# Optimization experiments

Measured on AMD Instinct MI355X. Metric: run time of the kernel, lower is better.

## Reference

```python
import jax, jax.numpy as jnp
import numpy as np

DIM = 768
NUM_HEADS = 12
HIDDEN = int(DIM * 4.0)
EPS = 1e-5


def setup_inputs() -> dict:
    key = jax.random.key(0)
    ks = jax.random.split(key, 8)
    s = lambda k, shape, scale=0.02: jax.random.normal(k, shape, dtype=jnp.float32) * scale
    return {
        "x": jax.random.normal(ks[0], (8, 1024, DIM), dtype=jnp.float32),
        "ln1_g": jnp.ones((DIM,), jnp.float32),
        "ln1_b": jnp.zeros((DIM,), jnp.float32),
        "qkv_w": s(ks[1], (DIM, 3 * DIM)),
        "qkv_b": jnp.zeros((3 * DIM,), jnp.float32),
        "proj_w": s(ks[2], (DIM, DIM)),
        "proj_b": jnp.zeros((DIM,), jnp.float32),
        "ln2_g": jnp.ones((DIM,), jnp.float32),
        "ln2_b": jnp.zeros((DIM,), jnp.float32),
        "fc1_w": s(ks[3], (DIM, HIDDEN)),
        "fc1_b": jnp.zeros((HIDDEN,), jnp.float32),
        "fc2_w": s(ks[4], (HIDDEN, DIM)),
        "fc2_b": jnp.zeros((DIM,), jnp.float32),
    }


def layer_norm(x, g, b):
    mu = jnp.mean(x, axis=-1, keepdims=True)
    var = jnp.mean(jnp.square(x - mu), axis=-1, keepdims=True)
    return (x - mu) * jax.lax.rsqrt(var + EPS) * g + b


def reference(x, ln1_g, ln1_b, qkv_w, qkv_b, proj_w, proj_b,
              ln2_g, ln2_b, fc1_w, fc1_b, fc2_w, fc2_b):
    B, N, C = x.shape
    H = NUM_HEADS
    Dh = C // H
    scale = Dh ** -0.5

    # --- Attention (pre-norm) ---
    h = layer_norm(x, ln1_g, ln1_b)
    qkv = h @ qkv_w + qkv_b                       # [B, N, 3C]
    qkv = qkv.reshape(B, N, 3, H, Dh)
    q, k, v = qkv[:, :, 0], qkv[:, :, 1], qkv[:, :, 2]  # [B, N, H, Dh]
    attn = jnp.einsum("bqhd,bkhd->bhqk", q, k) * scale  # [B, H, N, N]
    attn = jax.nn.softmax(attn, axis=-1)
    o = jnp.einsum("bhqk,bkhd->bqhd", attn, v).reshape(B, N, C)
    x = x + (o @ proj_w + proj_b)

    # --- MLP (pre-norm) ---
    h = layer_norm(x, ln2_g, ln2_b)
    h = jax.nn.gelu(h @ fc1_w + fc1_b, approximate=False)  # torch nn.GELU = exact erf
    x = x + (h @ fc2_w + fc2_b)
    return x
```

## Files before the change

kernel.cpp:

```cpp
#include <hip/hip_runtime.h>
#include <hip/hip_bf16.h>
#include <cstdint>

using f32x4   = __attribute__((ext_vector_type(4))) float;
using f32x16  = __attribute__((ext_vector_type(16))) float;
using bf16x8  = __attribute__((ext_vector_type(8))) short;

__device__ inline ushort f2bf(float f) {
    union { float f; uint u; } x; x.f = f;
    uint u = x.u;
    return (ushort)((u + 0x7FFFu + ((u >> 16) & 1u)) >> 16);
}

__device__ inline void gload16(const ushort* g, ushort* lds) {
    __builtin_amdgcn_global_load_lds(
        (const __attribute__((address_space(1))) unsigned int*)g,
        (__attribute__((address_space(3))) unsigned int*)lds, 16, 0, 0);
}

__device__ inline void transpose_body(const float* __restrict__ w,
                                      ushort* __restrict__ wt,
                                      int K, int N, int bx, int by,
                                      float (*tile)[33]) {
    const int bn = bx * 32, bk = by * 32;
    const int tx = threadIdx.x & 31, ty = threadIdx.x >> 5;
#pragma unroll
    for (int i = 0; i < 32; i += 8)
        tile[ty + i][tx] = w[(size_t)(bk + ty + i) * N + bn + tx];
    __syncthreads();
#pragma unroll
    for (int i = 0; i < 32; i += 8)
        wt[(size_t)(bn + ty + i) * K + bk + tx] = f2bf(tile[tx][ty + i]);
}

__device__ inline void ln_body(const float* __restrict__ x,
                               const float* __restrict__ g,
                               const float* __restrict__ b,
                               ushort* __restrict__ out, int row,
                               float* sa, float* sb) {
    const float* xr = x + (size_t)row * 768;
    const int t = threadIdx.x;
    float v0 = xr[t], v1 = xr[t + 256], v2 = xr[t + 512];
    float s  = v0 + v1 + v2;
    float sq = v0 * v0 + v1 * v1 + v2 * v2;
#pragma unroll
    for (int off = 32; off > 0; off >>= 1) {
        s  += __shfl_down(s, off);
        sq += __shfl_down(sq, off);
    }
    const int wv = t >> 6, lane = t & 63;
    if (lane == 0) { sa[wv] = s; sb[wv] = sq; }
    __syncthreads();
    s  = sa[0] + sa[1] + sa[2] + sa[3];
    sq = sb[0] + sb[1] + sb[2] + sb[3];
    const float mu   = s * (1.0f / 768.0f);
    const float var  = sq * (1.0f / 768.0f) - mu * mu;
    const float rstd = rsqrtf(var + 1e-5f);
    ushort* orow = out + (size_t)row * 768;
    orow[t]       = f2bf((v0 - mu) * rstd * g[t]       + b[t]);
    orow[t + 256] = f2bf((v1 - mu) * rstd * g[t + 256] + b[t + 256]);
    orow[t + 512] = f2bf((v2 - mu) * rstd * g[t + 512] + b[t + 512]);
}

__global__ __launch_bounds__(256) void prep(const float* __restrict__ qkv_w,
                                            const float* __restrict__ proj_w,
                                            const float* __restrict__ fc1_w,
                                            const float* __restrict__ fc2_w,
                                            ushort* __restrict__ qkv_wt,
                                            ushort* __restrict__ proj_wt,
                                            ushort* __restrict__ fc1_wt,
                                            ushort* __restrict__ fc2_wt,
                                            const float* __restrict__ x,
                                            const float* __restrict__ ln1_g,
                                            const float* __restrict__ ln1_b,
                                            ushort* __restrict__ hb) {
    __shared__ float tile[32][33];
    __shared__ float sa[4], sb[4];
    int blk = blockIdx.x;
    if (blk < 1728)      transpose_body(qkv_w, qkv_wt, 768, 2304, blk % 72, blk / 72, tile);
    else if (blk < 2304) { blk -= 1728; transpose_body(proj_w, proj_wt, 768, 768,  blk % 24, blk / 24, tile); }
    else if (blk < 4608) { blk -= 2304; transpose_body(fc1_w,  fc1_wt,  768, 3072, blk % 96, blk / 96, tile); }
    else if (blk < 6912) { blk -= 4608; transpose_body(fc2_w,  fc2_wt,  3072, 768, blk % 24, blk / 24, tile); }
    else                 ln_body(x, ln1_g, ln1_b, hb, blk - 6912, sa, sb);
}

__global__ __launch_bounds__(256) void ln_bf16(const float* __restrict__ x,
                                               const float* __restrict__ g,
                                               const float* __restrict__ b,
                                               ushort* __restrict__ out) {
    __shared__ float sa[4], sb[4];
    ln_body(x, g, b, out, blockIdx.x, sa, sb);
}

template <int EPI, int SWZ>
__global__ __launch_bounds__(256) void gemm_bt(const ushort* __restrict__ A,
                                               const ushort* __restrict__ Bt,
                                               const float* __restrict__ bias,
                                               const float* __restrict__ resid,
                                               void* __restrict__ out,
                                               void* __restrict__ out2,
                                               int M, int N, int K, int gx) {
    __shared__ ushort As[3][128 * 32];
    __shared__ ushort Bs[3][128 * 32];
    int bm, bn;
    if (SWZ) {
        const int bid = blockIdx.x;
        const int x = bid & 7, s = bid >> 3;
        bm = ((s / gx) * 8 + x) * 128;
        bn = (s % gx) * 128;
    } else {
        bm = blockIdx.y * 128;
        bn = blockIdx.x * 128;
    }
    const int t    = threadIdx.x;
    const int lane = t & 63;
    const int w    = t >> 6;
    const int wr   = w >> 1, wc = w & 1;
    const int lr   = lane >> 4, lc = lane & 15;

    const f32x4 fzero = {0.f, 0.f, 0.f, 0.f};
    f32x4 acc[4][4];
#pragma unroll
    for (int ai = 0; ai < 4; ++ai)
#pragma unroll
        for (int bj = 0; bj < 4; ++bj) acc[ai][bj] = fzero;

    const int srow = lane >> 2;
    const int sk8  = (lane & 3) * 8;
    const ushort* Ag0 = A  + (size_t)(bm + w * 16 + srow) * K + sk8;
    const ushort* Ag1 = Ag0 + (size_t)64 * K;
    const ushort* Bg0 = Bt + (size_t)(bn + w * 16 + srow) * K + sk8;
    const ushort* Bg1 = Bg0 + (size_t)64 * K;
    const int lo0 = (w * 16) * 32, lo1 = (64 + w * 16) * 32;

    const int nt = K >> 5;
    auto issue = [&](int tile, int buf) {
        const int kb = tile << 5;
        gload16(Ag0 + kb, &As[buf][lo0]);
        gload16(Ag1 + kb, &As[buf][lo1]);
        gload16(Bg0 + kb, &Bs[buf][lo0]);
        gload16(Bg1 + kb, &Bs[buf][lo1]);
    };
    issue(0, 0);
    if (nt > 1) issue(1, 1);

    for (int tk = 0; tk < nt; ++tk) {
        if (tk + 1 < nt) asm volatile("s_waitcnt vmcnt(4)" ::: "memory");
        else             asm volatile("s_waitcnt vmcnt(0)" ::: "memory");
        __builtin_amdgcn_sched_barrier(0);
        __builtin_amdgcn_s_barrier();
        __builtin_amdgcn_sched_barrier(0);
        if (tk + 2 < nt) issue(tk + 2, (tk + 2) % 3);
        const int cb = tk % 3;
        bf16x8 af[4], bf[4];
#pragma unroll
        for (int ai = 0; ai < 4; ++ai)
            af[ai] = *(const bf16x8*)&As[cb][(wr * 64 + ai * 16 + lc) * 32 + lr * 8];
#pragma unroll
        for (int bj = 0; bj < 4; ++bj)
            bf[bj] = *(const bf16x8*)&Bs[cb][(wc * 64 + bj * 16 + lc) * 32 + lr * 8];
#pragma unroll
        for (int ai = 0; ai < 4; ++ai)
#pragma unroll
            for (int bj = 0; bj < 4; ++bj)
                acc[ai][bj] = __builtin_amdgcn_mfma_f32_16x16x32_bf16(af[ai], bf[bj],
                                                                      acc[ai][bj], 0, 0, 0);
    }

#pragma unroll
    for (int ai = 0; ai < 4; ++ai) {
#pragma unroll
        for (int bj = 0; bj < 4; ++bj) {
            int col  = bn + wc * 64 + bj * 16 + lc;
            float bs = bias[col];
            if (EPI == 3 && col >= 1536) {
                int row0 = bm + wr * 64 + ai * 16 + lr * 4;
                int bb   = row0 >> 10, key0 = row0 & 1023;
                int c    = col - 1536;
                int h    = c >> 6, d = c & 63;
                ushort4 pk;
                pk.x = f2bf(acc[ai][bj][0] + bs);
                pk.y = f2bf(acc[ai][bj][1] + bs);
                pk.z = f2bf(acc[ai][bj][2] + bs);
                pk.w = f2bf(acc[ai][bj][3] + bs);
                *(ushort4*)((ushort*)out2 +
                            ((size_t)(bb * 12 + h) * 64 + d) * 1024 + key0) = pk;
                continue;
            }
            const float qsc = (EPI == 3 && col < 768) ? 0.125f : 1.0f;
#pragma unroll
            for (int j = 0; j < 4; ++j) {
                int row   = bm + wr * 64 + ai * 16 + lr * 4 + j;
                float val = acc[ai][bj][j] + bs;
                if (EPI == 1) {
                    val += resid[(size_t)row * N + col];
                    ((float*)out)[(size_t)row * N + col] = val;
                } else if (EPI == 2) {
                    val = 0.5f * val * (1.0f + erff(val * 0.70710678118f));
                    ((ushort*)out)[(size_t)row * N + col] = f2bf(val);
                } else {
                    ((ushort*)out)[(size_t)row * N + col] = f2bf(val * qsc);
                }
            }
        }
    }
}

__global__ __launch_bounds__(256) void attn_mfma(const ushort* __restrict__ qkv,
                                                 const ushort* __restrict__ vT,
                                                 ushort* __restrict__ outb) {
    __shared__ ushort Kls[64 * 72];
    __shared__ ushort Vtls[64 * 72];

    const int bid = blockIdx.x;
    const int b   = bid / 96;
    const int rem = bid % 96;
    const int h   = rem >> 3;
    const int qc  = rem & 7;
    const int t    = threadIdx.x;
    const int w    = t >> 6;
    const int lane = t & 63;
    const int l31  = lane & 31;
    const int hi   = lane >> 5;
    const int q0   = qc * 128 + w * 32;
    const size_t bbase = (size_t)b * 1024;
    const ushort* vTh = vT + ((size_t)(b * 12 + h) * 64) * 1024;

    bf16x8 qb[4];
    {
        const size_t qrow = (bbase + q0 + l31) * 2304 + h * 64;
#pragma unroll
        for (int dblk = 0; dblk < 4; ++dblk)
            qb[dblk] = *(const bf16x8*)(qkv + qrow + dblk * 16 + hi * 8);
    }

    f32x16 O[2];
#pragma unroll
    for (int ob = 0; ob < 2; ++ob)
#pragma unroll
        for (int r = 0; r < 16; ++r) O[ob][r] = 0.0f;
    float l = 0.0f;

    for (int kt = 0; kt < 16; ++kt) {
        const int k0 = kt * 64;
        __syncthreads();
#pragma unroll
        for (int i = 0; i < 2; ++i) {
            int idx = t + i * 256;
            int key = idx >> 3, seg = idx & 7;
            uint4 u = *(const uint4*)(qkv + (bbase + k0 + key) * 2304 + 768 +
                                      h * 64 + seg * 8);
            *(uint4*)&Kls[key * 72 + seg * 8] = u;
        }
#pragma unroll
        for (int i = 0; i < 2; ++i) {
            int idx = t + i * 256;
            int d = idx >> 3, seg = idx & 7;
            uint4 u = *(const uint4*)(vTh + (size_t)d * 1024 + k0 + seg * 8);
            *(uint4*)&Vtls[d * 72 + seg * 8] = u;
        }
        __syncthreads();

        f32x16 s[2];
#pragma unroll
        for (int kb = 0; kb < 2; ++kb) {
            f32x16 acc;
#pragma unroll
            for (int r = 0; r < 16; ++r) acc[r] = 0.0f;
#pragma unroll
            for (int dblk = 0; dblk < 4; ++dblk) {
                bf16x8 ka = *(const bf16x8*)&Kls[(kb * 32 + l31) * 72 + dblk * 16 + hi * 8];
                acc = __builtin_amdgcn_mfma_f32_32x32x16_bf16(ka, qb[dblk], acc, 0, 0, 0);
            }
            s[kb] = acc;
        }

        float psum = 0.0f;
#pragma unroll
        for (int kb = 0; kb < 2; ++kb)
#pragma unroll
            for (int r = 0; r < 16; ++r) {
                float p = __expf(s[kb][r]);
                s[kb][r] = p;
                psum += p;
            }
        psum += __shfl_xor(psum, 32);
        l += psum;

        bf16x8 pb[4];
#pragma unroll
        for (int kb16 = 0; kb16 < 4; ++kb16) {
            const int sb = kb16 >> 1, r0 = (kb16 & 1) * 8;
            uint own01 = (uint)f2bf(s[sb][r0 + 0]) | ((uint)f2bf(s[sb][r0 + 1]) << 16);
            uint own23 = (uint)f2bf(s[sb][r0 + 2]) | ((uint)f2bf(s[sb][r0 + 3]) << 16);
            uint own45 = (uint)f2bf(s[sb][r0 + 4]) | ((uint)f2bf(s[sb][r0 + 5]) << 16);
            uint own67 = (uint)f2bf(s[sb][r0 + 6]) | ((uint)f2bf(s[sb][r0 + 7]) << 16);
            uint sw01 = __shfl_xor(own01, 32);
            uint sw23 = __shfl_xor(own23, 32);
            uint sw45 = __shfl_xor(own45, 32);
            uint sw67 = __shfl_xor(own67, 32);
            uint d0 = hi ? sw45 : own01;
            uint d1 = hi ? sw67 : own23;
            uint d2 = hi ? own45 : sw01;
            uint d3 = hi ? own67 : sw23;
            union { uint u[4]; bf16x8 v; } cvt;
            cvt.u[0] = d0; cvt.u[1] = d1; cvt.u[2] = d2; cvt.u[3] = d3;
            pb[kb16] = cvt.v;
        }

#pragma unroll
        for (int ob = 0; ob < 2; ++ob)
#pragma unroll
            for (int kb16 = 0; kb16 < 4; ++kb16) {
                bf16x8 va = *(const bf16x8*)&Vtls[(ob * 32 + l31) * 72 + kb16 * 16 + hi * 8];
                O[ob] = __builtin_amdgcn_mfma_f32_32x32x16_bf16(va, pb[kb16], O[ob], 0, 0, 0);
            }
    }

    const float inv = 1.0f / l;
    ushort* orow = outb + (bbase + q0 + l31) * 768 + h * 64;
#pragma unroll
    for (int ob = 0; ob < 2; ++ob)
#pragma unroll
        for (int qd = 0; qd < 4; ++qd) {
            ushort4 pk;
            pk.x = f2bf(O[ob][qd * 4 + 0] * inv);
            pk.y = f2bf(O[ob][qd * 4 + 1] * inv);
            pk.z = f2bf(O[ob][qd * 4 + 2] * inv);
            pk.w = f2bf(O[ob][qd * 4 + 3] * inv);
            *(ushort4*)(orow + ob * 32 + qd * 8 + hi * 4) = pk;
        }
}

extern "C" void kernel_launch(void* const* d_in, const int* in_sizes, int n_in,
                              void* d_out, int out_size, void* d_ws, size_t ws_size,
                              hipStream_t stream) {
    const float* x      = (const float*)d_in[0];
    const float* ln1_g  = (const float*)d_in[1];
    const float* ln1_b  = (const float*)d_in[2];
    const float* qkv_w  = (const float*)d_in[3];
    const float* qkv_b  = (const float*)d_in[4];
    const float* proj_w = (const float*)d_in[5];
    const float* proj_b = (const float*)d_in[6];
    const float* ln2_g  = (const float*)d_in[7];
    const float* ln2_b  = (const float*)d_in[8];
    const float* fc1_w  = (const float*)d_in[9];
    const float* fc1_b  = (const float*)d_in[10];
    const float* fc2_w  = (const float*)d_in[11];
    const float* fc2_b  = (const float*)d_in[12];

    char* ws = (char*)d_ws;
    auto alloc = [&](size_t bytes) {
        char* p = ws;
        ws += (bytes + 255) & ~(size_t)255;
        return p;
    };
    ushort* qkv_wt  = (ushort*)alloc((size_t)768 * 2304 * 2);
    ushort* proj_wt = (ushort*)alloc((size_t)768 * 768 * 2);
    ushort* fc1_wt  = (ushort*)alloc((size_t)768 * 3072 * 2);
    ushort* fc2_wt  = (ushort*)alloc((size_t)3072 * 768 * 2);
    ushort* hb      = (ushort*)alloc((size_t)8192 * 768 * 2);
    ushort* qkvb    = (ushort*)alloc((size_t)8192 * 2304 * 2);
    ushort* vTb     = (ushort*)alloc((size_t)96 * 64 * 1024 * 2);
    ushort* ob      = (ushort*)alloc((size_t)8192 * 768 * 2);
    float*  x1      = (float*)alloc((size_t)8192 * 768 * 4);
    ushort* h2b     = (ushort*)alloc((size_t)8192 * 768 * 2);
    ushort* h3b     = (ushort*)alloc((size_t)8192 * 3072 * 2);

    prep<<<15104, 256, 0, stream>>>(qkv_w, proj_w, fc1_w, fc2_w,
                                    qkv_wt, proj_wt, fc1_wt, fc2_wt,
                                    x, ln1_g, ln1_b, hb);
    gemm_bt<3, 1><<<18 * 64, 256, 0, stream>>>(
        hb, qkv_wt, qkv_b, nullptr, qkvb, vTb, 8192, 2304, 768, 18);
    attn_mfma<<<768, 256, 0, stream>>>(qkvb, vTb, ob);
    gemm_bt<1, 1><<<6 * 64, 256, 0, stream>>>(
        ob, proj_wt, proj_b, x, x1, nullptr, 8192, 768, 768, 6);
    ln_bf16<<<8192, 256, 0, stream>>>(x1, ln2_g, ln2_b, h2b);
    gemm_bt<2, 1><<<24 * 64, 256, 0, stream>>>(
        h2b, fc1_wt, fc1_b, nullptr, h3b, nullptr, 8192, 3072, 768, 24);
    gemm_bt<1, 1><<<6 * 64, 256, 0, stream>>>(
        h3b, fc2_wt, fc2_b, x1, (float*)d_out, nullptr, 8192, 768, 3072, 6);
}
```

Before: 287.2 us.

## Use single-wave 64x64 triple-buffered GEMM kernel for fc1 with GELU epilogue

Adds a new GEMM kernel where each 64-thread block computes a 64x64 output tile using triple-buffered direct-to-LDS global loads and 16x16x32 bf16 MFMA, then uses it for the fc1+GELU GEMM instead of the 256-thread gemm_bt kernel. The aim is higher occupancy and more blocks (6144 vs 1536) to keep the GPU filled, with latency hiding through the 3-stage pipeline. In exchange, the smaller tiles lower data reuse per block and increase global/L2 traffic, and the LDS reads may have bank conflicts because the layout has no padding.

```diff
diff --git a/kernel.cpp b/kernel.cpp
--- a/kernel.cpp
+++ b/kernel.cpp
@@ -206,6 +206,89 @@
     }
 }
 
+template <int EPI>
+__global__ __launch_bounds__(64) void gemm_sw(const ushort* __restrict__ A,
+                                              const ushort* __restrict__ Bt,
+                                              const float* __restrict__ bias,
+                                              void* __restrict__ out,
+                                              int M, int N, int K, int gx) {
+    __shared__ ushort As[3][64 * 32];
+    __shared__ ushort Bs[3][64 * 32];
+    const int bid = blockIdx.x;
+    const int x = bid & 7, s = bid >> 3;
+    const int bm = ((s / gx) * 8 + x) * 64;
+    const int bn = (s % gx) * 64;
+    const int lane = threadIdx.x;
+    const int lr = lane >> 4, lc = lane & 15;
+    const int srow = lane >> 2, sk8 = (lane & 3) * 8;
+
+    const f32x4 fzero = {0.f, 0.f, 0.f, 0.f};
+    f32x4 acc[4][4];
+#pragma unroll
+    for (int ai = 0; ai < 4; ++ai)
+#pragma unroll
+        for (int bj = 0; bj < 4; ++bj) acc[ai][bj] = fzero;
+
+    const ushort* Ag[4];
+    const ushort* Bg[4];
+#pragma unroll
+    for (int i = 0; i < 4; ++i) {
+        Ag[i] = A  + (size_t)(bm + i * 16 + srow) * K + sk8;
+        Bg[i] = Bt + (size_t)(bn + i * 16 + srow) * K + sk8;
+    }
+
+    const int nt = K >> 5;
+    auto issue = [&](int tile, int buf) {
+        const int kb = tile << 5;
+#pragma unroll
+        for (int i = 0; i < 4; ++i) gload16(Ag[i] + kb, &As[buf][i * 512]);
+#pragma unroll
+        for (int i = 0; i < 4; ++i) gload16(Bg[i] + kb, &Bs[buf][i * 512]);
+    };
+    issue(0, 0);
+    issue(1, 1);
+
+    for (int tk = 0; tk < nt; ++tk) {
+        if (tk + 1 < nt) asm volatile("s_waitcnt vmcnt(8)" ::: "memory");
+        else             asm volatile("s_waitcnt vmcnt(0)" ::: "memory");
+        __builtin_amdgcn_sched_barrier(0);
+        asm volatile("s_waitcnt lgkmcnt(0)" ::: "memory");
+        __builtin_amdgcn_sched_barrier(0);
+        if (tk + 2 < nt) issue(tk + 2, (tk + 2) % 3);
+        const int cb = tk % 3;
+        bf16x8 af[4], bf[4];
+#pragma unroll
+        for (int ai = 0; ai < 4; ++ai)
+            af[ai] = *(const bf16x8*)&As[cb][(ai * 16 + lc) * 32 + lr * 8];
+#pragma unroll
+        for (int bj = 0; bj < 4; ++bj)
+            bf[bj] = *(const bf16x8*)&Bs[cb][(bj * 16 + lc) * 32 + lr * 8];
+#pragma unroll
+        for (int ai = 0; ai < 4; ++ai)
+#pragma unroll
+            for (int bj = 0; bj < 4; ++bj)
+                acc[ai][bj] = __builtin_amdgcn_mfma_f32_16x16x32_bf16(af[ai], bf[bj],
+                                                                      acc[ai][bj], 0, 0, 0);
+    }
+
+#pragma unroll
+    for (int ai = 0; ai < 4; ++ai) {
+#pragma unroll
+        for (int bj = 0; bj < 4; ++bj) {
+            int col  = bn + bj * 16 + lc;
+            float bs = bias[col];
+#pragma unroll
+            for (int j = 0; j < 4; ++j) {
+                int row   = bm + ai * 16 + lr * 4 + j;
+                float val = acc[ai][bj][j] + bs;
+                if (EPI == 2)
+                    val = 0.5f * val * (1.0f + erff(val * 0.70710678118f));
+                ((ushort*)out)[(size_t)row * N + col] = f2bf(val);
+            }
+        }
+    }
+}
+
 __global__ __launch_bounds__(256) void attn_mfma(const ushort* __restrict__ qkv,
                                                  const ushort* __restrict__ vT,
                                                  ushort* __restrict__ outb) {
@@ -376,8 +459,8 @@
     gemm_bt<1, 1><<<6 * 64, 256, 0, stream>>>(
         ob, proj_wt, proj_b, x, x1, nullptr, 8192, 768, 768, 6);
     ln_bf16<<<8192, 256, 0, stream>>>(x1, ln2_g, ln2_b, h2b);
-    gemm_bt<2, 1><<<24 * 64, 256, 0, stream>>>(
-        h2b, fc1_wt, fc1_b, nullptr, h3b, nullptr, 8192, 3072, 768, 24);
+    gemm_sw<2><<<128 * 48, 64, 0, stream>>>(
+        h2b, fc1_wt, fc1_b, h3b, 8192, 3072, 768, 48);
     gemm_bt<1, 1><<<6 * 64, 256, 0, stream>>>(
         h3b, fc2_wt, fc2_b, x1, (float*)d_out, nullptr, 8192, 768, 3072, 6);
 }
```

Result: slower. 326.3 us (+13.6%).
